# Optimization experiments

Measured on AMD Instinct MI355X. Metric: run time of the kernel, lower is better.

The kernel has to match this reference:

```python
import jax, jax.numpy as jnp
import numpy as np

N = 50000        # nodes
E = 800000       # edges (before self-loops)
IN = 512         # in_channels
HEADS = 8        # 'head' arg: heads and per-head out dim of conv1
C1 = 8           # per-head channels of conv1 (== head)
OUT = 128        # out_channels of conv2
NEG_SLOPE = 0.2  # PyG GATConv leaky-relu slope


def _glorot(key, shape, fan_in):
    return jax.random.normal(key, shape, jnp.float32) * (1.0 / np.sqrt(fan_in))


def setup_inputs() -> dict:
    key = jax.random.key(0)
    ks = jax.random.split(key, 10)
    x = jax.random.normal(ks[0], (N, IN), jnp.float32)
    edge_index = jax.random.randint(ks[1], (2, E), 0, N, dtype=jnp.int32)
    # conv1: GATConv(IN, C1, heads=HEADS, concat=True)
    W1 = _glorot(ks[2], (IN, HEADS * C1), IN)
    att_src1 = _glorot(ks[3], (HEADS, C1), C1)
    att_dst1 = _glorot(ks[4], (HEADS, C1), C1)
    bias1 = jnp.zeros((HEADS * C1,), jnp.float32)
    # conv2: GATConv(HEADS*C1, OUT, heads=1, concat=False)
    W2 = _glorot(ks[5], (HEADS * C1, OUT), HEADS * C1)
    att_src2 = _glorot(ks[6], (1, OUT), OUT)
    att_dst2 = _glorot(ks[7], (1, OUT), OUT)
    bias2 = jnp.zeros((OUT,), jnp.float32)
    return {"x": x, "edge_index": edge_index,
            "W1": W1, "att_src1": att_src1, "att_dst1": att_dst1, "bias1": bias1,
            "W2": W2, "att_src2": att_src2, "att_dst2": att_dst2, "bias2": bias2}


def gat_conv(x, src, dst, W, a_src, a_dst, bias, heads, concat):
    """PyG GATConv (eval mode, dropout off). src/dst already include self-loops."""
    n = x.shape[0]
    h = (x @ W).reshape(n, heads, -1)                 # [N, H, C]
    s = (h * a_src[None]).sum(-1)                     # [N, H] alpha_src per node
    d = (h * a_dst[None]).sum(-1)                     # [N, H] alpha_dst per node
    alpha = jax.nn.leaky_relu(s[src] + d[dst], NEG_SLOPE)  # [E, H]
    # segment softmax over incoming edges of each destination node
    amax = jax.ops.segment_max(alpha, dst, num_segments=n)  # [N, H]
    amax = jnp.where(jnp.isfinite(amax), amax, 0.0)
    ea = jnp.exp(alpha - amax[dst])                   # [E, H]
    denom = jax.ops.segment_sum(ea, dst, num_segments=n)
    w = ea / (denom[dst] + 1e-16)                     # [E, H]
    msg = h[src] * w[..., None]                       # [E, H, C]
    out = jax.ops.segment_sum(msg, dst, num_segments=n)  # [N, H, C]
    out = out.reshape(n, -1) if concat else out.mean(axis=1)
    return out + bias


def reference(x, edge_index, W1, att_src1, att_dst1, bias1,
              W2, att_src2, att_dst2, bias2):
    n = x.shape[0]
    loop = jnp.arange(n, dtype=edge_index.dtype)      # PyG adds self-loops
    src = jnp.concatenate([edge_index[0], loop])
    dst = jnp.concatenate([edge_index[1], loop])
    h = jax.nn.elu(gat_conv(x, src, dst, W1, att_src1, att_dst1, bias1,
                            heads=HEADS, concat=True))
    out = jax.nn.elu(gat_conv(h, src, dst, W2, att_src2, att_dst2, bias2,
                              heads=1, concat=False))
    return out
```

## Files before the change

kernel.cpp:

```cpp
#include <hip/hip_runtime.h>

#define NEG_SLOPE 0.2f

typedef __attribute__((ext_vector_type(8))) short bf16x8;
typedef __attribute__((ext_vector_type(4))) float f32x4;

__device__ __forceinline__ float leaky(float v) {
    return v > 0.0f ? v : NEG_SLOPE * v;
}
__device__ __forceinline__ float elu(float v) {
    return v > 0.0f ? v : (__expf(v) - 1.0f);
}
__device__ __forceinline__ short f2b(float f) {
    return (short)((__float_as_uint(f) + 0x8000u) >> 16);
}
__device__ __forceinline__ float bf2f(unsigned short v) {
    return __uint_as_float(((unsigned)v) << 16);
}

__global__ void prep_k(const float* __restrict__ W1, const float* __restrict__ W2,
                       unsigned short* __restrict__ w1s, unsigned short* __restrict__ w2s,
                       int* __restrict__ deg, int N) {
    int i = blockIdx.x * 256 + threadIdx.x;
    if (i < N) deg[i] = 0;
    if (i < 512 * 64) {
        int k = i >> 6, n = i & 63;
        int kt = k >> 5, kk = k & 31;
        int nt = n >> 4, nn = n & 15;
        int lane = (kk >> 3) * 16 + nn, j = kk & 7;
        w1s[(((size_t)(kt * 4 + nt)) * 64 + lane) * 8 + j] = (unsigned short)f2b(W1[i]);
    } else if (i < 512 * 64 + 64 * 128) {
        int i2 = i - 512 * 64;
        int k = i2 >> 7, n = i2 & 127;
        int kt = k >> 5, kk = k & 31;
        int nt = n >> 4, nn = n & 15;
        int lane = (kk >> 3) * 16 + nn, j = kk & 7;
        w2s[(((size_t)(kt * 8 + nt)) * 64 + lane) * 8 + j] = (unsigned short)f2b(W2[i2]);
    }
}

__global__ __launch_bounds__(256) void gemm1_k(const float* __restrict__ X,
                                               const unsigned short* __restrict__ Ws,
                                               const float* __restrict__ Asrc,
                                               const float* __restrict__ Adst,
                                               unsigned short* __restrict__ Hb,
                                               float* __restrict__ S,
                                               float* __restrict__ D, int N) {
    const int lane = threadIdx.x & 63;
    const int wave = threadIdx.x >> 6;
    const int m0 = blockIdx.x * 64 + wave * 16;
    const int q = lane >> 4, lc = lane & 15;
    const int arow = m0 + lc;
    const float* xrow = X + (size_t)min(arow, N - 1) * 512 + q * 8;
    const bf16x8* bW = (const bf16x8*)Ws;

    f32x4 acc[4] = {{0.f,0.f,0.f,0.f},{0.f,0.f,0.f,0.f},{0.f,0.f,0.f,0.f},{0.f,0.f,0.f,0.f}};

    for (int kt = 0; kt < 16; ++kt) {
        float4 a0 = *(const float4*)(xrow + kt * 32);
        float4 a1 = *(const float4*)(xrow + kt * 32 + 4);
        bf16x8 af;
        af[0] = f2b(a0.x); af[1] = f2b(a0.y); af[2] = f2b(a0.z); af[3] = f2b(a0.w);
        af[4] = f2b(a1.x); af[5] = f2b(a1.y); af[6] = f2b(a1.z); af[7] = f2b(a1.w);
#pragma unroll
        for (int nt = 0; nt < 4; ++nt) {
            bf16x8 bf = bW[(size_t)(kt * 4 + nt) * 64 + lane];
            acc[nt] = __builtin_amdgcn_mfma_f32_16x16x32_bf16(af, bf, acc[nt], 0, 0, 0);
        }
    }

    float asc[4], adc[4];
#pragma unroll
    for (int nt = 0; nt < 4; ++nt) { asc[nt] = Asrc[nt * 16 + lc]; adc[nt] = Adst[nt * 16 + lc]; }

#pragma unroll
    for (int r = 0; r < 4; ++r) {
        int row = m0 + q * 4 + r;
        bool ok = row < N;
        if (ok) {
#pragma unroll
            for (int nt = 0; nt < 4; ++nt)
                Hb[(size_t)row * 64 + nt * 16 + lc] = (unsigned short)f2b(acc[nt][r]);
        }
        float ps[4], pd[4];
#pragma unroll
        for (int nt = 0; nt < 4; ++nt) { ps[nt] = acc[nt][r] * asc[nt]; pd[nt] = acc[nt][r] * adc[nt]; }
#pragma unroll
        for (int off = 1; off < 8; off <<= 1) {
#pragma unroll
            for (int nt = 0; nt < 4; ++nt) {
                ps[nt] += __shfl_xor(ps[nt], off);
                pd[nt] += __shfl_xor(pd[nt], off);
            }
        }
        if (ok && !(lc & 7)) {
            int hb = lc >> 3;
#pragma unroll
            for (int nt = 0; nt < 4; ++nt) {
                S[(size_t)row * 8 + nt * 2 + hb] = ps[nt];
                D[(size_t)row * 8 + nt * 2 + hb] = pd[nt];
            }
        }
    }
}

__global__ __launch_bounds__(256) void gemm2_k(const unsigned short* __restrict__ X,
                                               const unsigned short* __restrict__ Ws,
                                               const float* __restrict__ Asrc,
                                               const float* __restrict__ Adst,
                                               unsigned short* __restrict__ Hb,
                                               float* __restrict__ S,
                                               float* __restrict__ D, int N) {
    const int lane = threadIdx.x & 63;
    const int wave = threadIdx.x >> 6;
    const int m0 = blockIdx.x * 64 + wave * 16;
    const int q = lane >> 4, lc = lane & 15;
    const int arow = m0 + lc;
    const unsigned short* xrow = X + (size_t)min(arow, N - 1) * 64 + q * 8;
    const bf16x8* bW = (const bf16x8*)Ws;

    f32x4 acc[8] = {{0.f,0.f,0.f,0.f},{0.f,0.f,0.f,0.f},{0.f,0.f,0.f,0.f},{0.f,0.f,0.f,0.f},
                    {0.f,0.f,0.f,0.f},{0.f,0.f,0.f,0.f},{0.f,0.f,0.f,0.f},{0.f,0.f,0.f,0.f}};

#pragma unroll
    for (int kt = 0; kt < 2; ++kt) {
        bf16x8 af = *(const bf16x8*)(xrow + kt * 32);
#pragma unroll
        for (int nt = 0; nt < 8; ++nt) {
            bf16x8 bf = bW[(size_t)(kt * 8 + nt) * 64 + lane];
            acc[nt] = __builtin_amdgcn_mfma_f32_16x16x32_bf16(af, bf, acc[nt], 0, 0, 0);
        }
    }

    float asc[8], adc[8];
#pragma unroll
    for (int nt = 0; nt < 8; ++nt) { asc[nt] = Asrc[nt * 16 + lc]; adc[nt] = Adst[nt * 16 + lc]; }

#pragma unroll
    for (int r = 0; r < 4; ++r) {
        int row = m0 + q * 4 + r;
        bool ok = row < N;
        if (ok) {
#pragma unroll
            for (int nt = 0; nt < 8; ++nt)
                Hb[(size_t)row * 128 + nt * 16 + lc] = (unsigned short)f2b(acc[nt][r]);
        }
        float ps = 0.f, pd = 0.f;
#pragma unroll
        for (int nt = 0; nt < 8; ++nt) { ps += acc[nt][r] * asc[nt]; pd += acc[nt][r] * adc[nt]; }
#pragma unroll
        for (int off = 1; off < 16; off <<= 1) {
            ps += __shfl_xor(ps, off);
            pd += __shfl_xor(pd, off);
        }
        if (ok && lc == 0) { S[row] = ps; D[row] = pd; }
    }
}

__global__ void deg_k(const int* __restrict__ dst, int E, int* __restrict__ deg) {
    int base = (blockIdx.x * blockDim.x + threadIdx.x) * 8;
    if (base + 8 <= E) {
        int4 a = *(const int4*)(dst + base);
        int4 b = *(const int4*)(dst + base + 4);
        atomicAdd(&deg[a.x], 1); atomicAdd(&deg[a.y], 1);
        atomicAdd(&deg[a.z], 1); atomicAdd(&deg[a.w], 1);
        atomicAdd(&deg[b.x], 1); atomicAdd(&deg[b.y], 1);
        atomicAdd(&deg[b.z], 1); atomicAdd(&deg[b.w], 1);
    } else {
        for (int e = base; e < E; ++e) atomicAdd(&deg[dst[e]], 1);
    }
}

__global__ __launch_bounds__(256) void scanA_k(const int* __restrict__ deg,
                                               int* __restrict__ rowptr,
                                               int* __restrict__ partials, int N) {
    __shared__ int s[256];
    const int t = threadIdx.x;
    const int base = blockIdx.x * 1024;
    int v[4];
    int idx = base + t * 4;
#pragma unroll
    for (int i = 0; i < 4; ++i) v[i] = (idx + i < N) ? deg[idx + i] + 1 : 0;
    int sum = v[0] + v[1] + v[2] + v[3];
    s[t] = sum;
    __syncthreads();
    for (int off = 1; off < 256; off <<= 1) {
        int x = (t >= off) ? s[t - off] : 0;
        __syncthreads();
        s[t] += x;
        __syncthreads();
    }
    int run = s[t] - sum;
#pragma unroll
    for (int i = 0; i < 4; ++i) {
        if (idx + i < N) rowptr[idx + i] = run;
        run += v[i];
    }
    if (t == 255) partials[blockIdx.x] = s[255];
}

__global__ __launch_bounds__(256) void scanB_k(const int* __restrict__ partials,
                                               int* __restrict__ poff,
                                               int* __restrict__ rowptr, int nb,
                                               int N, int Etot) {
    __shared__ int s[256];
    const int t = threadIdx.x;
    int v = (t < nb) ? partials[t] : 0;
    s[t] = v;
    __syncthreads();
    for (int off = 1; off < 256; off <<= 1) {
        int x = (t >= off) ? s[t - off] : 0;
        __syncthreads();
        s[t] += x;
        __syncthreads();
    }
    poff[t] = s[t] - v;
    if (t == 0) rowptr[N] = Etot;
}

__global__ void scanC_k(int* __restrict__ rowptr, const int* __restrict__ poff,
                        int* __restrict__ wp, int* __restrict__ srcs, int N) {
    int i = blockIdx.x * blockDim.x + threadIdx.x;
    if (i >= N) return;
    int r = rowptr[i] + poff[i >> 10];
    rowptr[i] = r;
    srcs[r] = i;
    wp[i] = r + 1;
}

__global__ void scatter_k(const int* __restrict__ ei, int E,
                          int* __restrict__ wp, int* __restrict__ srcs) {
    int base = (blockIdx.x * blockDim.x + threadIdx.x) * 4;
    if (base + 4 <= E) {
        int4 s = *(const int4*)(ei + base);
        int4 d = *(const int4*)(ei + E + base);
        int p0 = atomicAdd(&wp[d.x], 1);
        int p1 = atomicAdd(&wp[d.y], 1);
        int p2 = atomicAdd(&wp[d.z], 1);
        int p3 = atomicAdd(&wp[d.w], 1);
        srcs[p0] = s.x; srcs[p1] = s.y; srcs[p2] = s.z; srcs[p3] = s.w;
    } else {
        for (int e = base; e < E; ++e) {
            int p = atomicAdd(&wp[ei[E + e]], 1);
            srcs[p] = ei[e];
        }
    }
}

__global__ __launch_bounds__(256) void agg1_csr_k(const int* __restrict__ rowptr,
                                                  const int* __restrict__ srcs,
                                                  const float* __restrict__ S,
                                                  const float* __restrict__ D,
                                                  const unsigned short* __restrict__ Hb,
                                                  const float* __restrict__ bias,
                                                  unsigned short* __restrict__ out, int N) {
    const int wid = (blockIdx.x * 256 + threadIdx.x) >> 6;
    const int lane = threadIdx.x & 63;
    if (wid >= N) return;
    const int beg = rowptr[wid], end = rowptr[wid + 1];
    const int h = lane & 7;
    const int el = lane >> 3;
    const float dvh = D[(size_t)wid * 8 + h];

    float m = -1e30f;
    for (int i = beg + el; i < end; i += 8)
        m = fmaxf(m, leaky(S[(size_t)srcs[i] * 8 + h] + dvh));
#pragma unroll
    for (int off = 8; off < 64; off <<= 1)
        m = fmaxf(m, __shfl_xor(m, off));

    float acc = 0.0f, den = 0.0f;
    for (int base = beg; base < end; base += 8) {
        int i = base + el;
        int src_l = 0; float w_l = 0.0f;
        if (i < end) {
            src_l = srcs[i];
            w_l = __expf(leaky(S[(size_t)src_l * 8 + h] + dvh) - m);
        }
        den += w_l;
#pragma unroll
        for (int j = 0; j < 8; ++j) {
            float w = __shfl(w_l, j * 8 + (lane >> 3));
            int src = __builtin_amdgcn_readfirstlane(__shfl(src_l, j * 8));
            acc += w * bf2f(Hb[(size_t)src * 64 + lane]);
        }
    }
#pragma unroll
    for (int off = 8; off < 64; off <<= 1)
        den += __shfl_xor(den, off);
    float rden = 1.0f / (__shfl(den, lane >> 3) + 1e-16f);
    out[(size_t)wid * 64 + lane] = (unsigned short)f2b(elu(acc * rden + bias[lane]));
}

__global__ __launch_bounds__(256) void agg2_csr_k(const int* __restrict__ rowptr,
                                                  const int* __restrict__ srcs,
                                                  const float* __restrict__ S,
                                                  const float* __restrict__ D,
                                                  const unsigned short* __restrict__ Hb,
                                                  const float* __restrict__ bias,
                                                  float* __restrict__ out, int N) {
    const int wid = (blockIdx.x * 256 + threadIdx.x) >> 6;
    const int lane = threadIdx.x & 63;
    if (wid >= N) return;
    const int beg = rowptr[wid], end = rowptr[wid + 1];
    const float dvh = D[wid];
    const int c0 = lane * 2;

    float m = -1e30f;
    for (int i = beg + lane; i < end; i += 64)
        m = fmaxf(m, leaky(S[srcs[i]] + dvh));
#pragma unroll
    for (int off = 1; off < 64; off <<= 1)
        m = fmaxf(m, __shfl_xor(m, off));

    float acc0 = 0.0f, acc1 = 0.0f, den = 0.0f;
    for (int base = beg; base < end; base += 64) {
        int i = base + lane;
        int src_l = 0; float w_l = 0.0f;
        if (i < end) {
            src_l = srcs[i];
            w_l = __expf(leaky(S[src_l] + dvh) - m);
        }
        den += w_l;
        const int cnt = min(64, end - base);
        for (int j0 = 0; j0 < cnt; j0 += 8) {
#pragma unroll
            for (int u = 0; u < 8; ++u) {
                int j = j0 + u;
                float w = __shfl(w_l, j);
                int src = __builtin_amdgcn_readfirstlane(__shfl(src_l, j));
                unsigned p = *(const unsigned*)(Hb + (size_t)src * 128 + c0);
                acc0 += w * __uint_as_float(p << 16);
                acc1 += w * __uint_as_float(p & 0xffff0000u);
            }
        }
    }
#pragma unroll
    for (int off = 1; off < 64; off <<= 1)
        den += __shfl_xor(den, off);
    const float rden = 1.0f / (den + 1e-16f);
    float2 o;
    o.x = elu(acc0 * rden + bias[c0]);
    o.y = elu(acc1 * rden + bias[c0 + 1]);
    *(float2*)(out + (size_t)wid * 128 + c0) = o;
}

extern "C" void kernel_launch(void* const* d_in, const int* in_sizes, int n_in,
                              void* d_out, int out_size, void* d_ws, size_t ws_size,
                              hipStream_t stream) {
    const float* x   = (const float*)d_in[0];
    const int*   ei  = (const int*)d_in[1];
    const float* W1  = (const float*)d_in[2];
    const float* as1 = (const float*)d_in[3];
    const float* ad1 = (const float*)d_in[4];
    const float* b1  = (const float*)d_in[5];
    const float* W2  = (const float*)d_in[6];
    const float* as2 = (const float*)d_in[7];
    const float* ad2 = (const float*)d_in[8];
    const float* b2  = (const float*)d_in[9];

    const int N = in_sizes[0] / 512;
    const int E = in_sizes[1] / 2;
    const int Etot = E + N;
    float* out = (float*)d_out;

    unsigned short* w1s    = (unsigned short*)d_ws;
    unsigned short* w2s    = w1s + 512 * 64;
    unsigned short* out1b  = w2s + 64 * 128;
    unsigned short* h1b    = out1b + (size_t)N * 64;
    float*          s1     = (float*)(h1b + (size_t)N * 64);
    float*          d1     = s1 + (size_t)N * 8;
    unsigned short* h2b    = (unsigned short*)(d1 + (size_t)N * 8);
    float*          s2     = (float*)(h2b + (size_t)N * 128);
    float*          d2     = s2 + N;
    int*            rowptr = (int*)(d2 + N);
    int*            srcs   = rowptr + (N + 1);
    int* deg      = (int*)h2b;
    int* wp       = deg + N;
    int* partials = wp + N;
    int* poff     = partials + 256;

    const int B = 256;
    const int nb = (N + 1023) / 1024;
    const int gblk = (N + 63) / 64;
    const int prep_n = (N > 512 * 64 + 64 * 128) ? N : (512 * 64 + 64 * 128);

    prep_k<<<(prep_n + B - 1) / B, B, 0, stream>>>(W1, W2, w1s, w2s, deg, N);
    deg_k<<<(E + B * 8 - 1) / (B * 8), B, 0, stream>>>(ei + E, E, deg);
    scanA_k<<<nb, B, 0, stream>>>(deg, rowptr, partials, N);
    scanB_k<<<1, B, 0, stream>>>(partials, poff, rowptr, nb, N, Etot);
    scanC_k<<<(N + B - 1) / B, B, 0, stream>>>(rowptr, poff, wp, srcs, N);
    scatter_k<<<(E + B * 4 - 1) / (B * 4), B, 0, stream>>>(ei, E, wp, srcs);

    gemm1_k<<<gblk, B, 0, stream>>>(x, w1s, as1, ad1, h1b, s1, d1, N);
    agg1_csr_k<<<(N + 3) / 4, B, 0, stream>>>(rowptr, srcs, s1, d1, h1b, b1, out1b, N);

    gemm2_k<<<gblk, B, 0, stream>>>(out1b, w2s, as2, ad2, h2b, s2, d2, N);
    agg2_csr_k<<<(N + 3) / 4, B, 0, stream>>>(rowptr, srcs, s2, d2, h2b, b2, out, N);
}
```

Baseline: 364.8 us.

## Restructure GAT aggregation to per-lane edge groups with 16-byte row loads

Both aggregation kernels now give each lane group its own edge and have each lane load 8 bf16 features with one vector load. This replaces the earlier scheme where every edge was broadcast through shuffles and readfirstlane and each lane loaded one or two elements. Partial sums are combined with a cross-group shuffle reduction at the end, and only one group writes vectorized output. The row max is now taken over raw source scores with leaky applied once afterwards, which is valid because leaky is monotonic. In exchange, each lane holds 8 accumulators and the end of each node pays extra shuffle reductions.

```diff
diff --git a/kernel.cpp b/kernel.cpp
--- a/kernel.cpp
+++ b/kernel.cpp
@@ -259,37 +259,45 @@
     if (wid >= N) return;
     const int beg = rowptr[wid], end = rowptr[wid + 1];
     const int h = lane & 7;
-    const int el = lane >> 3;
+    const int eg = lane >> 3;
     const float dvh = D[(size_t)wid * 8 + h];
 
-    float m = -1e30f;
-    for (int i = beg + el; i < end; i += 8)
-        m = fmaxf(m, leaky(S[(size_t)srcs[i] * 8 + h] + dvh));
+    float ms = -1e30f;
+    for (int i = beg + eg; i < end; i += 8)
+        ms = fmaxf(ms, S[(size_t)srcs[i] * 8 + h]);
 #pragma unroll
     for (int off = 8; off < 64; off <<= 1)
-        m = fmaxf(m, __shfl_xor(m, off));
-
-    float acc = 0.0f, den = 0.0f;
+        ms = fmaxf(ms, __shfl_xor(ms, off));
+    const float m = leaky(ms + dvh);
+
+    float acc[8] = {0.f,0.f,0.f,0.f,0.f,0.f,0.f,0.f};
+    float den = 0.0f;
     for (int base = beg; base < end; base += 8) {
-        int i = base + el;
-        int src_l = 0; float w_l = 0.0f;
-        if (i < end) {
-            src_l = srcs[i];
-            w_l = __expf(leaky(S[(size_t)src_l * 8 + h] + dvh) - m);
-        }
-        den += w_l;
-#pragma unroll
-        for (int j = 0; j < 8; ++j) {
-            float w = __shfl(w_l, j * 8 + (lane >> 3));
-            int src = __builtin_amdgcn_readfirstlane(__shfl(src_l, j * 8));
-            acc += w * bf2f(Hb[(size_t)src * 64 + lane]);
-        }
-    }
-#pragma unroll
-    for (int off = 8; off < 64; off <<= 1)
+        int i = base + eg;
+        bool v = i < end;
+        int src = v ? srcs[i] : wid;
+        float w = v ? __expf(leaky(S[(size_t)src * 8 + h] + dvh) - m) : 0.0f;
+        den += w;
+        bf16x8 hv = *(const bf16x8*)(Hb + (size_t)src * 64 + h * 8);
+#pragma unroll
+        for (int c = 0; c < 8; ++c)
+            acc[c] += w * bf2f((unsigned short)hv[c]);
+    }
+#pragma unroll
+    for (int off = 8; off < 64; off <<= 1) {
         den += __shfl_xor(den, off);
-    float rden = 1.0f / (__shfl(den, lane >> 3) + 1e-16f);
-    out[(size_t)wid * 64 + lane] = (unsigned short)f2b(elu(acc * rden + bias[lane]));
+#pragma unroll
+        for (int c = 0; c < 8; ++c)
+            acc[c] += __shfl_xor(acc[c], off);
+    }
+    if (eg == 0) {
+        const float rden = 1.0f / (den + 1e-16f);
+        bf16x8 o;
+#pragma unroll
+        for (int c = 0; c < 8; ++c)
+            o[c] = f2b(elu(acc[c] * rden + bias[h * 8 + c]));
+        *(bf16x8*)(out + (size_t)wid * 64 + h * 8) = o;
+    }
 }
 
 __global__ __launch_bounds__(256) void agg2_csr_k(const int* __restrict__ rowptr,
@@ -303,46 +311,54 @@
     const int lane = threadIdx.x & 63;
     if (wid >= N) return;
     const int beg = rowptr[wid], end = rowptr[wid + 1];
-    const float dvh = D[wid];
-    const int c0 = lane * 2;
-
-    float m = -1e30f;
+    const int eg = lane >> 4;
+    const int sl = lane & 15;
+    const float dv = D[wid];
+
+    float ms = -1e30f;
     for (int i = beg + lane; i < end; i += 64)
-        m = fmaxf(m, leaky(S[srcs[i]] + dvh));
+        ms = fmaxf(ms, S[srcs[i]]);
 #pragma unroll
     for (int off = 1; off < 64; off <<= 1)
-        m = fmaxf(m, __shfl_xor(m, off));
-
-    float acc0 = 0.0f, acc1 = 0.0f, den = 0.0f;
-    for (int base = beg; base < end; base += 64) {
-        int i = base + lane;
-        int src_l = 0; float w_l = 0.0f;
-        if (i < end) {
-            src_l = srcs[i];
-            w_l = __expf(leaky(S[src_l] + dvh) - m);
-        }
-        den += w_l;
-        const int cnt = min(64, end - base);
-        for (int j0 = 0; j0 < cnt; j0 += 8) {
-#pragma unroll
-            for (int u = 0; u < 8; ++u) {
-                int j = j0 + u;
-                float w = __shfl(w_l, j);
-                int src = __builtin_amdgcn_readfirstlane(__shfl(src_l, j));
-                unsigned p = *(const unsigned*)(Hb + (size_t)src * 128 + c0);
-                acc0 += w * __uint_as_float(p << 16);
-                acc1 += w * __uint_as_float(p & 0xffff0000u);
-            }
-        }
+        ms = fmaxf(ms, __shfl_xor(ms, off));
+    const float m = leaky(ms + dv);
+
+    float acc[8] = {0.f,0.f,0.f,0.f,0.f,0.f,0.f,0.f};
+    float den = 0.0f;
+    for (int base = beg; base < end; base += 4) {
+        int i = base + eg;
+        bool v = i < end;
+        int src = v ? srcs[i] : wid;
+        float w = v ? __expf(leaky(S[src] + dv) - m) : 0.0f;
+        den += w;
+        bf16x8 hv = *(const bf16x8*)(Hb + (size_t)src * 128 + sl * 8);
+#pragma unroll
+        for (int c = 0; c < 8; ++c)
+            acc[c] += w * bf2f((unsigned short)hv[c]);
     }
 #pragma unroll
     for (int off = 1; off < 64; off <<= 1)
         den += __shfl_xor(den, off);
-    const float rden = 1.0f / (den + 1e-16f);
-    float2 o;
-    o.x = elu(acc0 * rden + bias[c0]);
-    o.y = elu(acc1 * rden + bias[c0 + 1]);
-    *(float2*)(out + (size_t)wid * 128 + c0) = o;
+#pragma unroll
+    for (int off = 16; off < 64; off <<= 1) {
+#pragma unroll
+        for (int c = 0; c < 8; ++c)
+            acc[c] += __shfl_xor(acc[c], off);
+    }
+    if (eg == 0) {
+        const float rden = 1.0f / (den * 0.0625f + 1e-16f);
+        float4 o0, o1;
+        o0.x = elu(acc[0] * rden + bias[sl * 8 + 0]);
+        o0.y = elu(acc[1] * rden + bias[sl * 8 + 1]);
+        o0.z = elu(acc[2] * rden + bias[sl * 8 + 2]);
+        o0.w = elu(acc[3] * rden + bias[sl * 8 + 3]);
+        o1.x = elu(acc[4] * rden + bias[sl * 8 + 4]);
+        o1.y = elu(acc[5] * rden + bias[sl * 8 + 5]);
+        o1.z = elu(acc[6] * rden + bias[sl * 8 + 6]);
+        o1.w = elu(acc[7] * rden + bias[sl * 8 + 7]);
+        *(float4*)(out + (size_t)wid * 128 + sl * 8) = o0;
+        *(float4*)(out + (size_t)wid * 128 + sl * 8 + 4) = o1;
+    }
 }
 
 extern "C" void kernel_launch(void* const* d_in, const int* in_sizes, int n_in,
```

After: 378.0 us. 3.6% more time.

## Fuse whole GAT pipeline into one persistent cooperative kernel with grid syncs

Applied to the files above, without the earlier changes.

Replaces the ten separate kernel launches with one persistent cooperative kernel that steps through phases separated by grid.sync, sized from occupancy. The degree count is overlapped with the first GEMM in the same phase. The three-kernel scan is collapsed into one pass that takes chunk offsets with an atomic, and rowptr becomes beg plus deg. The aim is to remove launch gaps and tail effects, at the cost of grid-wide barriers, a fixed persistent grid that may limit latency hiding in the gather phases, and a launch_bounds of 4 that may constrain registers.

```diff
diff --git a/kernel.cpp b/kernel.cpp
--- a/kernel.cpp
+++ b/kernel.cpp
@@ -1,4 +1,7 @@
 #include <hip/hip_runtime.h>
+#include <hip/hip_cooperative_groups.h>
+
+namespace cg = cooperative_groups;
 
 #define NEG_SLOPE 0.2f
 
@@ -18,331 +21,312 @@
     return __uint_as_float(((unsigned)v) << 16);
 }
 
-__global__ void prep_k(const float* __restrict__ W1, const float* __restrict__ W2,
-                       unsigned short* __restrict__ w1s, unsigned short* __restrict__ w2s,
-                       int* __restrict__ deg, int N) {
-    int i = blockIdx.x * 256 + threadIdx.x;
-    if (i < N) deg[i] = 0;
-    if (i < 512 * 64) {
-        int k = i >> 6, n = i & 63;
-        int kt = k >> 5, kk = k & 31;
-        int nt = n >> 4, nn = n & 15;
-        int lane = (kk >> 3) * 16 + nn, j = kk & 7;
-        w1s[(((size_t)(kt * 4 + nt)) * 64 + lane) * 8 + j] = (unsigned short)f2b(W1[i]);
-    } else if (i < 512 * 64 + 64 * 128) {
-        int i2 = i - 512 * 64;
-        int k = i2 >> 7, n = i2 & 127;
-        int kt = k >> 5, kk = k & 31;
-        int nt = n >> 4, nn = n & 15;
-        int lane = (kk >> 3) * 16 + nn, j = kk & 7;
-        w2s[(((size_t)(kt * 8 + nt)) * 64 + lane) * 8 + j] = (unsigned short)f2b(W2[i2]);
-    }
-}
-
-__global__ __launch_bounds__(256) void gemm1_k(const float* __restrict__ X,
-                                               const unsigned short* __restrict__ Ws,
-                                               const float* __restrict__ Asrc,
-                                               const float* __restrict__ Adst,
-                                               unsigned short* __restrict__ Hb,
-                                               float* __restrict__ S,
-                                               float* __restrict__ D, int N) {
-    const int lane = threadIdx.x & 63;
-    const int wave = threadIdx.x >> 6;
-    const int m0 = blockIdx.x * 64 + wave * 16;
-    const int q = lane >> 4, lc = lane & 15;
-    const int arow = m0 + lc;
-    const float* xrow = X + (size_t)min(arow, N - 1) * 512 + q * 8;
-    const bf16x8* bW = (const bf16x8*)Ws;
-
-    f32x4 acc[4] = {{0.f,0.f,0.f,0.f},{0.f,0.f,0.f,0.f},{0.f,0.f,0.f,0.f},{0.f,0.f,0.f,0.f}};
-
-    for (int kt = 0; kt < 16; ++kt) {
-        float4 a0 = *(const float4*)(xrow + kt * 32);
-        float4 a1 = *(const float4*)(xrow + kt * 32 + 4);
-        bf16x8 af;
-        af[0] = f2b(a0.x); af[1] = f2b(a0.y); af[2] = f2b(a0.z); af[3] = f2b(a0.w);
-        af[4] = f2b(a1.x); af[5] = f2b(a1.y); af[6] = f2b(a1.z); af[7] = f2b(a1.w);
-#pragma unroll
-        for (int nt = 0; nt < 4; ++nt) {
-            bf16x8 bf = bW[(size_t)(kt * 4 + nt) * 64 + lane];
-            acc[nt] = __builtin_amdgcn_mfma_f32_16x16x32_bf16(af, bf, acc[nt], 0, 0, 0);
+struct GP {
+    const float* x; const int* ei;
+    const float* W1; const float* as1; const float* ad1; const float* b1;
+    const float* W2; const float* as2; const float* ad2; const float* b2;
+    unsigned short* w1s; unsigned short* w2s;
+    unsigned short* out1b; unsigned short* h1b; unsigned short* h2b;
+    float* s1; float* d1; float* s2; float* d2;
+    int* beg; int* deg; int* wp; int* srcs;
+    float* out;
+    int N; int E;
+};
+
+__global__ __launch_bounds__(256, 4) void fused_k(GP p, int plo, int phi) {
+    cg::grid_group grid = cg::this_grid();
+    const int tid  = threadIdx.x;
+    const int bid  = blockIdx.x;
+    const int nB   = gridDim.x;
+    const int gsz  = nB * 256;
+    const int gtid = bid * 256 + tid;
+    const int lane = tid & 63;
+    const int wave = tid >> 6;
+    const int N = p.N, E = p.E;
+    const int gblk = (N + 63) >> 6;
+    const int nb   = (N + 1023) >> 10;
+    const int nW   = gsz >> 6;
+    const int gw   = gtid >> 6;
+
+    __shared__ int sm[256];
+    __shared__ int chunkBase;
+
+    for (int ph = plo; ph <= phi; ++ph) {
+        switch (ph) {
+        case 0: {
+            for (int i = gtid; i < 512 * 64 + 64 * 128; i += gsz) {
+                if (i < 512 * 64) {
+                    int k = i >> 6, n = i & 63;
+                    int kt = k >> 5, kk = k & 31;
+                    int nt = n >> 4, nn = n & 15;
+                    int l = (kk >> 3) * 16 + nn, j = kk & 7;
+                    p.w1s[(((size_t)(kt * 4 + nt)) * 64 + l) * 8 + j] = (unsigned short)f2b(p.W1[i]);
+                } else {
+                    int i2 = i - 512 * 64;
+                    int k = i2 >> 7, n = i2 & 127;
+                    int kt = k >> 5, kk = k & 31;
+                    int nt = n >> 4, nn = n & 15;
+                    int l = (kk >> 3) * 16 + nn, j = kk & 7;
+                    p.w2s[(((size_t)(kt * 8 + nt)) * 64 + l) * 8 + j] = (unsigned short)f2b(p.W2[i2]);
+                }
+            }
+            for (int i = gtid; i <= N; i += gsz) p.deg[i] = 0;
+        } break;
+
+        case 1: {
+            for (int base = gtid * 8; base < E; base += gsz * 8) {
+                if (base + 8 <= E) {
+                    int4 a = *(const int4*)(p.ei + E + base);
+                    int4 b = *(const int4*)(p.ei + E + base + 4);
+                    atomicAdd(&p.deg[a.x], 1); atomicAdd(&p.deg[a.y], 1);
+                    atomicAdd(&p.deg[a.z], 1); atomicAdd(&p.deg[a.w], 1);
+                    atomicAdd(&p.deg[b.x], 1); atomicAdd(&p.deg[b.y], 1);
+                    atomicAdd(&p.deg[b.z], 1); atomicAdd(&p.deg[b.w], 1);
+                } else {
+                    for (int e = base; e < E; ++e) atomicAdd(&p.deg[p.ei[E + e]], 1);
+                }
+            }
+            const int q = lane >> 4, lc = lane & 15;
+            const bf16x8* bW = (const bf16x8*)p.w1s;
+            for (int t = bid; t < gblk; t += nB) {
+                const int m0 = t * 64 + wave * 16;
+                const int arow = m0 + lc;
+                const float* xrow = p.x + (size_t)min(arow, N - 1) * 512 + q * 8;
+
+                f32x4 acc[4] = {{0.f,0.f,0.f,0.f},{0.f,0.f,0.f,0.f},{0.f,0.f,0.f,0.f},{0.f,0.f,0.f,0.f}};
+                for (int kt = 0; kt < 16; ++kt) {
+                    float4 a0 = *(const float4*)(xrow + kt * 32);
+                    float4 a1 = *(const float4*)(xrow + kt * 32 + 4);
+                    bf16x8 af;
+                    af[0] = f2b(a0.x); af[1] = f2b(a0.y); af[2] = f2b(a0.z); af[3] = f2b(a0.w);
+                    af[4] = f2b(a1.x); af[5] = f2b(a1.y); af[6] = f2b(a1.z); af[7] = f2b(a1.w);
+#pragma unroll
+                    for (int nt = 0; nt < 4; ++nt) {
+                        bf16x8 bf = bW[(size_t)(kt * 4 + nt) * 64 + lane];
+                        acc[nt] = __builtin_amdgcn_mfma_f32_16x16x32_bf16(af, bf, acc[nt], 0, 0, 0);
+                    }
+                }
+                float asc[4], adc[4];
+#pragma unroll
+                for (int nt = 0; nt < 4; ++nt) { asc[nt] = p.as1[nt * 16 + lc]; adc[nt] = p.ad1[nt * 16 + lc]; }
+#pragma unroll
+                for (int r = 0; r < 4; ++r) {
+                    int row = m0 + q * 4 + r;
+                    bool ok = row < N;
+                    if (ok) {
+#pragma unroll
+                        for (int nt = 0; nt < 4; ++nt)
+                            p.h1b[(size_t)row * 64 + nt * 16 + lc] = (unsigned short)f2b(acc[nt][r]);
+                    }
+                    float ps[4], pd[4];
+#pragma unroll
+                    for (int nt = 0; nt < 4; ++nt) { ps[nt] = acc[nt][r] * asc[nt]; pd[nt] = acc[nt][r] * adc[nt]; }
+#pragma unroll
+                    for (int off = 1; off < 8; off <<= 1) {
+#pragma unroll
+                        for (int nt = 0; nt < 4; ++nt) {
+                            ps[nt] += __shfl_xor(ps[nt], off);
+                            pd[nt] += __shfl_xor(pd[nt], off);
+                        }
+                    }
+                    if (ok && !(lc & 7)) {
+                        int hb = lc >> 3;
+#pragma unroll
+                        for (int nt = 0; nt < 4; ++nt) {
+                            p.s1[(size_t)row * 8 + nt * 2 + hb] = ps[nt];
+                            p.d1[(size_t)row * 8 + nt * 2 + hb] = pd[nt];
+                        }
+                    }
+                }
+            }
+        } break;
+
+        case 2: {
+            for (int c = nB - 1 - bid; c < nb; c += nB) {
+                int v[4];
+                int idx = c * 1024 + tid * 4;
+#pragma unroll
+                for (int i = 0; i < 4; ++i) v[i] = (idx + i < N) ? p.deg[idx + i] + 1 : 0;
+                int sum = v[0] + v[1] + v[2] + v[3];
+                sm[tid] = sum;
+                __syncthreads();
+                for (int off = 1; off < 256; off <<= 1) {
+                    int xv = (tid >= off) ? sm[tid - off] : 0;
+                    __syncthreads();
+                    sm[tid] += xv;
+                    __syncthreads();
+                }
+                if (tid == 255) chunkBase = atomicAdd(&p.deg[N], sm[255]);
+                __syncthreads();
+                int run = chunkBase + sm[tid] - sum;
+#pragma unroll
+                for (int i = 0; i < 4; ++i) {
+                    if (idx + i < N) {
+                        p.beg[idx + i] = run;
+                        p.srcs[run] = idx + i;
+                        p.wp[idx + i] = run + 1;
+                        run += v[i];
+                    }
+                }
+                __syncthreads();
+            }
+        } break;
+
+        case 3: {
+            for (int base = gtid * 4; base < E; base += gsz * 4) {
+                if (base + 4 <= E) {
+                    int4 s = *(const int4*)(p.ei + base);
+                    int4 d = *(const int4*)(p.ei + E + base);
+                    int p0 = atomicAdd(&p.wp[d.x], 1);
+                    int p1 = atomicAdd(&p.wp[d.y], 1);
+                    int p2 = atomicAdd(&p.wp[d.z], 1);
+                    int p3 = atomicAdd(&p.wp[d.w], 1);
+                    p.srcs[p0] = s.x; p.srcs[p1] = s.y; p.srcs[p2] = s.z; p.srcs[p3] = s.w;
+                } else {
+                    for (int e = base; e < E; ++e) {
+                        int pp = atomicAdd(&p.wp[p.ei[E + e]], 1);
+                        p.srcs[pp] = p.ei[e];
+                    }
+                }
+            }
+        } break;
+
+        case 4: {
+            for (int wid = gw; wid < N; wid += nW) {
+                const int b0 = p.beg[wid];
+                const int e0 = b0 + p.deg[wid] + 1;
+                const int h = lane & 7;
+                const int el = lane >> 3;
+                const float dvh = p.d1[(size_t)wid * 8 + h];
+
+                float m = -1e30f;
+                for (int i = b0 + el; i < e0; i += 8)
+                    m = fmaxf(m, leaky(p.s1[(size_t)p.srcs[i] * 8 + h] + dvh));
+#pragma unroll
+                for (int off = 8; off < 64; off <<= 1)
+                    m = fmaxf(m, __shfl_xor(m, off));
+
+                float acc = 0.0f, den = 0.0f;
+                for (int base = b0; base < e0; base += 8) {
+                    int i = base + el;
+                    int src_l = 0; float w_l = 0.0f;
+                    if (i < e0) {
+                        src_l = p.srcs[i];
+                        w_l = __expf(leaky(p.s1[(size_t)src_l * 8 + h] + dvh) - m);
+                    }
+                    den += w_l;
+#pragma unroll
+                    for (int j = 0; j < 8; ++j) {
+                        float w = __shfl(w_l, j * 8 + (lane >> 3));
+                        int src = __builtin_amdgcn_readfirstlane(__shfl(src_l, j * 8));
+                        acc += w * bf2f(p.h1b[(size_t)src * 64 + lane]);
+                    }
+                }
+#pragma unroll
+                for (int off = 8; off < 64; off <<= 1)
+                    den += __shfl_xor(den, off);
+                float rden = 1.0f / (__shfl(den, lane >> 3) + 1e-16f);
+                p.out1b[(size_t)wid * 64 + lane] = (unsigned short)f2b(elu(acc * rden + p.b1[lane]));
+            }
+        } break;
+
+        case 5: {
+            const int q = lane >> 4, lc = lane & 15;
+            const bf16x8* bW = (const bf16x8*)p.w2s;
+            for (int t = bid; t < gblk; t += nB) {
+                const int m0 = t * 64 + wave * 16;
+                const int arow = m0 + lc;
+                const unsigned short* xrow = p.out1b + (size_t)min(arow, N - 1) * 64 + q * 8;
+
+                f32x4 acc[8] = {{0.f,0.f,0.f,0.f},{0.f,0.f,0.f,0.f},{0.f,0.f,0.f,0.f},{0.f,0.f,0.f,0.f},
+                                {0.f,0.f,0.f,0.f},{0.f,0.f,0.f,0.f},{0.f,0.f,0.f,0.f},{0.f,0.f,0.f,0.f}};
+#pragma unroll
+                for (int kt = 0; kt < 2; ++kt) {
+                    bf16x8 af = *(const bf16x8*)(xrow + kt * 32);
+#pragma unroll
+                    for (int nt = 0; nt < 8; ++nt) {
+                        bf16x8 bf = bW[(size_t)(kt * 8 + nt) * 64 + lane];
+                        acc[nt] = __builtin_amdgcn_mfma_f32_16x16x32_bf16(af, bf, acc[nt], 0, 0, 0);
+                    }
+                }
+                float asc[8], adc[8];
+#pragma unroll
+                for (int nt = 0; nt < 8; ++nt) { asc[nt] = p.as2[nt * 16 + lc]; adc[nt] = p.ad2[nt * 16 + lc]; }
+#pragma unroll
+                for (int r = 0; r < 4; ++r) {
+                    int row = m0 + q * 4 + r;
+                    bool ok = row < N;
+                    if (ok) {
+#pragma unroll
+                        for (int nt = 0; nt < 8; ++nt)
+                            p.h2b[(size_t)row * 128 + nt * 16 + lc] = (unsigned short)f2b(acc[nt][r]);
+                    }
+                    float ps = 0.f, pd = 0.f;
+#pragma unroll
+                    for (int nt = 0; nt < 8; ++nt) { ps += acc[nt][r] * asc[nt]; pd += acc[nt][r] * adc[nt]; }
+#pragma unroll
+                    for (int off = 1; off < 16; off <<= 1) {
+                        ps += __shfl_xor(ps, off);
+                        pd += __shfl_xor(pd, off);
+                    }
+                    if (ok && lc == 0) { p.s2[row] = ps; p.d2[row] = pd; }
+                }
+            }
+        } break;
+
+        case 6: {
+            for (int wid = gw; wid < N; wid += nW) {
+                const int b0 = p.beg[wid];
+                const int e0 = b0 + p.deg[wid] + 1;
+                const float dv = p.d2[wid];
+                const int c0 = lane * 2;
+
+                float m = -1e30f;
+                for (int i = b0 + lane; i < e0; i += 64)
+                    m = fmaxf(m, leaky(p.s2[p.srcs[i]] + dv));
+#pragma unroll
+                for (int off = 1; off < 64; off <<= 1)
+                    m = fmaxf(m, __shfl_xor(m, off));
+
+                float acc0 = 0.0f, acc1 = 0.0f, den = 0.0f;
+                for (int base = b0; base < e0; base += 64) {
+                    int i = base + lane;
+                    int src_l = 0; float w_l = 0.0f;
+                    if (i < e0) {
+                        src_l = p.srcs[i];
+                        w_l = __expf(leaky(p.s2[src_l] + dv) - m);
+                    }
+                    den += w_l;
+                    const int cnt = min(64, e0 - base);
+                    for (int j0 = 0; j0 < cnt; j0 += 8) {
+#pragma unroll
+                        for (int u = 0; u < 8; ++u) {
+                            int j = j0 + u;
+                            float w = __shfl(w_l, j);
+                            int src = __builtin_amdgcn_readfirstlane(__shfl(src_l, j));
+                            unsigned pv = *(const unsigned*)(p.h2b + (size_t)src * 128 + c0);
+                            acc0 += w * __uint_as_float(pv << 16);
+                            acc1 += w * __uint_as_float(pv & 0xffff0000u);
+                        }
+                    }
+                }
+#pragma unroll
+                for (int off = 1; off < 64; off <<= 1)
+                    den += __shfl_xor(den, off);
+                const float rden = 1.0f / (den + 1e-16f);
+                float2 o;
+                o.x = elu(acc0 * rden + p.b2[c0]);
+                o.y = elu(acc1 * rden + p.b2[c0 + 1]);
+                *(float2*)(p.out + (size_t)wid * 128 + c0) = o;
+            }
+        } break;
+        }
+
+        if (ph < phi) {
+            __threadfence();
+            grid.sync();
         }
     }
-
-    float asc[4], adc[4];
-#pragma unroll
-    for (int nt = 0; nt < 4; ++nt) { asc[nt] = Asrc[nt * 16 + lc]; adc[nt] = Adst[nt * 16 + lc]; }
-
-#pragma unroll
-    for (int r = 0; r < 4; ++r) {
-        int row = m0 + q * 4 + r;
-        bool ok = row < N;
-        if (ok) {
-#pragma unroll
-            for (int nt = 0; nt < 4; ++nt)
-                Hb[(size_t)row * 64 + nt * 16 + lc] = (unsigned short)f2b(acc[nt][r]);
-        }
-        float ps[4], pd[4];
-#pragma unroll
-        for (int nt = 0; nt < 4; ++nt) { ps[nt] = acc[nt][r] * asc[nt]; pd[nt] = acc[nt][r] * adc[nt]; }
-#pragma unroll
-        for (int off = 1; off < 8; off <<= 1) {
-#pragma unroll
-            for (int nt = 0; nt < 4; ++nt) {
-                ps[nt] += __shfl_xor(ps[nt], off);
-                pd[nt] += __shfl_xor(pd[nt], off);
-            }
-        }
-        if (ok && !(lc & 7)) {
-            int hb = lc >> 3;
-#pragma unroll
-            for (int nt = 0; nt < 4; ++nt) {
-                S[(size_t)row * 8 + nt * 2 + hb] = ps[nt];
-                D[(size_t)row * 8 + nt * 2 + hb] = pd[nt];
-            }
-        }
-    }
-}
-
-__global__ __launch_bounds__(256) void gemm2_k(const unsigned short* __restrict__ X,
-                                               const unsigned short* __restrict__ Ws,
-                                               const float* __restrict__ Asrc,
-                                               const float* __restrict__ Adst,
-                                               unsigned short* __restrict__ Hb,
-                                               float* __restrict__ S,
-                                               float* __restrict__ D, int N) {
-    const int lane = threadIdx.x & 63;
-    const int wave = threadIdx.x >> 6;
-    const int m0 = blockIdx.x * 64 + wave * 16;
-    const int q = lane >> 4, lc = lane & 15;
-    const int arow = m0 + lc;
-    const unsigned short* xrow = X + (size_t)min(arow, N - 1) * 64 + q * 8;
-    const bf16x8* bW = (const bf16x8*)Ws;
-
-    f32x4 acc[8] = {{0.f,0.f,0.f,0.f},{0.f,0.f,0.f,0.f},{0.f,0.f,0.f,0.f},{0.f,0.f,0.f,0.f},
-                    {0.f,0.f,0.f,0.f},{0.f,0.f,0.f,0.f},{0.f,0.f,0.f,0.f},{0.f,0.f,0.f,0.f}};
-
-#pragma unroll
-    for (int kt = 0; kt < 2; ++kt) {
-        bf16x8 af = *(const bf16x8*)(xrow + kt * 32);
-#pragma unroll
-        for (int nt = 0; nt < 8; ++nt) {
-            bf16x8 bf = bW[(size_t)(kt * 8 + nt) * 64 + lane];
-            acc[nt] = __builtin_amdgcn_mfma_f32_16x16x32_bf16(af, bf, acc[nt], 0, 0, 0);
-        }
-    }
-
-    float asc[8], adc[8];
-#pragma unroll
-    for (int nt = 0; nt < 8; ++nt) { asc[nt] = Asrc[nt * 16 + lc]; adc[nt] = Adst[nt * 16 + lc]; }
-
-#pragma unroll
-    for (int r = 0; r < 4; ++r) {
-        int row = m0 + q * 4 + r;
-        bool ok = row < N;
-        if (ok) {
-#pragma unroll
-            for (int nt = 0; nt < 8; ++nt)
-                Hb[(size_t)row * 128 + nt * 16 + lc] = (unsigned short)f2b(acc[nt][r]);
-        }
-        float ps = 0.f, pd = 0.f;
-#pragma unroll
-        for (int nt = 0; nt < 8; ++nt) { ps += acc[nt][r] * asc[nt]; pd += acc[nt][r] * adc[nt]; }
-#pragma unroll
-        for (int off = 1; off < 16; off <<= 1) {
-            ps += __shfl_xor(ps, off);
-            pd += __shfl_xor(pd, off);
-        }
-        if (ok && lc == 0) { S[row] = ps; D[row] = pd; }
-    }
-}
-
-__global__ void deg_k(const int* __restrict__ dst, int E, int* __restrict__ deg) {
-    int base = (blockIdx.x * blockDim.x + threadIdx.x) * 8;
-    if (base + 8 <= E) {
-        int4 a = *(const int4*)(dst + base);
-        int4 b = *(const int4*)(dst + base + 4);
-        atomicAdd(&deg[a.x], 1); atomicAdd(&deg[a.y], 1);
-        atomicAdd(&deg[a.z], 1); atomicAdd(&deg[a.w], 1);
-        atomicAdd(&deg[b.x], 1); atomicAdd(&deg[b.y], 1);
-        atomicAdd(&deg[b.z], 1); atomicAdd(&deg[b.w], 1);
-    } else {
-        for (int e = base; e < E; ++e) atomicAdd(&deg[dst[e]], 1);
-    }
-}
-
-__global__ __launch_bounds__(256) void scanA_k(const int* __restrict__ deg,
-                                               int* __restrict__ rowptr,
-                                               int* __restrict__ partials, int N) {
-    __shared__ int s[256];
-    const int t = threadIdx.x;
-    const int base = blockIdx.x * 1024;
-    int v[4];
-    int idx = base + t * 4;
-#pragma unroll
-    for (int i = 0; i < 4; ++i) v[i] = (idx + i < N) ? deg[idx + i] + 1 : 0;
-    int sum = v[0] + v[1] + v[2] + v[3];
-    s[t] = sum;
-    __syncthreads();
-    for (int off = 1; off < 256; off <<= 1) {
-        int x = (t >= off) ? s[t - off] : 0;
-        __syncthreads();
-        s[t] += x;
-        __syncthreads();
-    }
-    int run = s[t] - sum;
-#pragma unroll
-    for (int i = 0; i < 4; ++i) {
-        if (idx + i < N) rowptr[idx + i] = run;
-        run += v[i];
-    }
-    if (t == 255) partials[blockIdx.x] = s[255];
-}
-
-__global__ __launch_bounds__(256) void scanB_k(const int* __restrict__ partials,
-                                               int* __restrict__ poff,
-                                               int* __restrict__ rowptr, int nb,
-                                               int N, int Etot) {
-    __shared__ int s[256];
-    const int t = threadIdx.x;
-    int v = (t < nb) ? partials[t] : 0;
-    s[t] = v;
-    __syncthreads();
-    for (int off = 1; off < 256; off <<= 1) {
-        int x = (t >= off) ? s[t - off] : 0;
-        __syncthreads();
-        s[t] += x;
-        __syncthreads();
-    }
-    poff[t] = s[t] - v;
-    if (t == 0) rowptr[N] = Etot;
-}
-
-__global__ void scanC_k(int* __restrict__ rowptr, const int* __restrict__ poff,
-                        int* __restrict__ wp, int* __restrict__ srcs, int N) {
-    int i = blockIdx.x * blockDim.x + threadIdx.x;
-    if (i >= N) return;
-    int r = rowptr[i] + poff[i >> 10];
-    rowptr[i] = r;
-    srcs[r] = i;
-    wp[i] = r + 1;
-}
-
-__global__ void scatter_k(const int* __restrict__ ei, int E,
-                          int* __restrict__ wp, int* __restrict__ srcs) {
-    int base = (blockIdx.x * blockDim.x + threadIdx.x) * 4;
-    if (base + 4 <= E) {
-        int4 s = *(const int4*)(ei + base);
-        int4 d = *(const int4*)(ei + E + base);
-        int p0 = atomicAdd(&wp[d.x], 1);
-        int p1 = atomicAdd(&wp[d.y], 1);
-        int p2 = atomicAdd(&wp[d.z], 1);
-        int p3 = atomicAdd(&wp[d.w], 1);
-        srcs[p0] = s.x; srcs[p1] = s.y; srcs[p2] = s.z; srcs[p3] = s.w;
-    } else {
-        for (int e = base; e < E; ++e) {
-            int p = atomicAdd(&wp[ei[E + e]], 1);
-            srcs[p] = ei[e];
-        }
-    }
-}
-
-__global__ __launch_bounds__(256) void agg1_csr_k(const int* __restrict__ rowptr,
-                                                  const int* __restrict__ srcs,
-                                                  const float* __restrict__ S,
-                                                  const float* __restrict__ D,
-                                                  const unsigned short* __restrict__ Hb,
-                                                  const float* __restrict__ bias,
-                                                  unsigned short* __restrict__ out, int N) {
-    const int wid = (blockIdx.x * 256 + threadIdx.x) >> 6;
-    const int lane = threadIdx.x & 63;
-    if (wid >= N) return;
-    const int beg = rowptr[wid], end = rowptr[wid + 1];
-    const int h = lane & 7;
-    const int el = lane >> 3;
-    const float dvh = D[(size_t)wid * 8 + h];
-
-    float m = -1e30f;
-    for (int i = beg + el; i < end; i += 8)
-        m = fmaxf(m, leaky(S[(size_t)srcs[i] * 8 + h] + dvh));
-#pragma unroll
-    for (int off = 8; off < 64; off <<= 1)
-        m = fmaxf(m, __shfl_xor(m, off));
-
-    float acc = 0.0f, den = 0.0f;
-    for (int base = beg; base < end; base += 8) {
-        int i = base + el;
-        int src_l = 0; float w_l = 0.0f;
-        if (i < end) {
-            src_l = srcs[i];
-            w_l = __expf(leaky(S[(size_t)src_l * 8 + h] + dvh) - m);
-        }
-        den += w_l;
-#pragma unroll
-        for (int j = 0; j < 8; ++j) {
-            float w = __shfl(w_l, j * 8 + (lane >> 3));
-            int src = __builtin_amdgcn_readfirstlane(__shfl(src_l, j * 8));
-            acc += w * bf2f(Hb[(size_t)src * 64 + lane]);
-        }
-    }
-#pragma unroll
-    for (int off = 8; off < 64; off <<= 1)
-        den += __shfl_xor(den, off);
-    float rden = 1.0f / (__shfl(den, lane >> 3) + 1e-16f);
-    out[(size_t)wid * 64 + lane] = (unsigned short)f2b(elu(acc * rden + bias[lane]));
-}
-
-__global__ __launch_bounds__(256) void agg2_csr_k(const int* __restrict__ rowptr,
-                                                  const int* __restrict__ srcs,
-                                                  const float* __restrict__ S,
-                                                  const float* __restrict__ D,
-                                                  const unsigned short* __restrict__ Hb,
-                                                  const float* __restrict__ bias,
-                                                  float* __restrict__ out, int N) {
-    const int wid = (blockIdx.x * 256 + threadIdx.x) >> 6;
-    const int lane = threadIdx.x & 63;
-    if (wid >= N) return;
-    const int beg = rowptr[wid], end = rowptr[wid + 1];
-    const float dvh = D[wid];
-    const int c0 = lane * 2;
-
-    float m = -1e30f;
-    for (int i = beg + lane; i < end; i += 64)
-        m = fmaxf(m, leaky(S[srcs[i]] + dvh));
-#pragma unroll
-    for (int off = 1; off < 64; off <<= 1)
-        m = fmaxf(m, __shfl_xor(m, off));
-
-    float acc0 = 0.0f, acc1 = 0.0f, den = 0.0f;
-    for (int base = beg; base < end; base += 64) {
-        int i = base + lane;
-        int src_l = 0; float w_l = 0.0f;
-        if (i < end) {
-            src_l = srcs[i];
-            w_l = __expf(leaky(S[src_l] + dvh) - m);
-        }
-        den += w_l;
-        const int cnt = min(64, end - base);
-        for (int j0 = 0; j0 < cnt; j0 += 8) {
-#pragma unroll
-            for (int u = 0; u < 8; ++u) {
-                int j = j0 + u;
-                float w = __shfl(w_l, j);
-                int src = __builtin_amdgcn_readfirstlane(__shfl(src_l, j));
-                unsigned p = *(const unsigned*)(Hb + (size_t)src * 128 + c0);
-                acc0 += w * __uint_as_float(p << 16);
-                acc1 += w * __uint_as_float(p & 0xffff0000u);
-            }
-        }
-    }
-#pragma unroll
-    for (int off = 1; off < 64; off <<= 1)
-        den += __shfl_xor(den, off);
-    const float rden = 1.0f / (den + 1e-16f);
-    float2 o;
-    o.x = elu(acc0 * rden + bias[c0]);
-    o.y = elu(acc1 * rden + bias[c0 + 1]);
-    *(float2*)(out + (size_t)wid * 128 + c0) = o;
 }
 
 extern "C" void kernel_launch(void* const* d_in, const int* in_sizes, int n_in,
@@ -361,40 +345,57 @@
 
     const int N = in_sizes[0] / 512;
     const int E = in_sizes[1] / 2;
-    const int Etot = E + N;
-    float* out = (float*)d_out;
-
-    unsigned short* w1s    = (unsigned short*)d_ws;
-    unsigned short* w2s    = w1s + 512 * 64;
-    unsigned short* out1b  = w2s + 64 * 128;
-    unsigned short* h1b    = out1b + (size_t)N * 64;
-    float*          s1     = (float*)(h1b + (size_t)N * 64);
-    float*          d1     = s1 + (size_t)N * 8;
-    unsigned short* h2b    = (unsigned short*)(d1 + (size_t)N * 8);
-    float*          s2     = (float*)(h2b + (size_t)N * 128);
-    float*          d2     = s2 + N;
-    int*            rowptr = (int*)(d2 + N);
-    int*            srcs   = rowptr + (N + 1);
-    int* deg      = (int*)h2b;
-    int* wp       = deg + N;
-    int* partials = wp + N;
-    int* poff     = partials + 256;
-
-    const int B = 256;
-    const int nb = (N + 1023) / 1024;
-    const int gblk = (N + 63) / 64;
-    const int prep_n = (N > 512 * 64 + 64 * 128) ? N : (512 * 64 + 64 * 128);
-
-    prep_k<<<(prep_n + B - 1) / B, B, 0, stream>>>(W1, W2, w1s, w2s, deg, N);
-    deg_k<<<(E + B * 8 - 1) / (B * 8), B, 0, stream>>>(ei + E, E, deg);
-    scanA_k<<<nb, B, 0, stream>>>(deg, rowptr, partials, N);
-    scanB_k<<<1, B, 0, stream>>>(partials, poff, rowptr, nb, N, Etot);
-    scanC_k<<<(N + B - 1) / B, B, 0, stream>>>(rowptr, poff, wp, srcs, N);
-    scatter_k<<<(E + B * 4 - 1) / (B * 4), B, 0, stream>>>(ei, E, wp, srcs);
-
-    gemm1_k<<<gblk, B, 0, stream>>>(x, w1s, as1, ad1, h1b, s1, d1, N);
-    agg1_csr_k<<<(N + 3) / 4, B, 0, stream>>>(rowptr, srcs, s1, d1, h1b, b1, out1b, N);
-
-    gemm2_k<<<gblk, B, 0, stream>>>(out1b, w2s, as2, ad2, h2b, s2, d2, N);
-    agg2_csr_k<<<(N + 3) / 4, B, 0, stream>>>(rowptr, srcs, s2, d2, h2b, b2, out, N);
-}
+
+    unsigned short* w1s   = (unsigned short*)d_ws;
+    unsigned short* w2s   = w1s + 512 * 64;
+    unsigned short* out1b = w2s + 64 * 128;
+    unsigned short* h1b   = out1b + (size_t)N * 64;
+    unsigned short* h2b   = h1b + (size_t)N * 64;
+    float*          s1    = (float*)(h2b + (size_t)N * 128);
+    float*          d1    = s1 + (size_t)N * 8;
+    float*          s2    = d1 + (size_t)N * 8;
+    float*          d2    = s2 + N;
+    int*            beg   = (int*)(d2 + N);
+    int*            deg   = beg + N;
+    int*            wp    = deg + (N + 1);
+    int*            srcs  = wp + N;
+
+    GP p;
+    p.x = x; p.ei = ei;
+    p.W1 = W1; p.as1 = as1; p.ad1 = ad1; p.b1 = b1;
+    p.W2 = W2; p.as2 = as2; p.ad2 = ad2; p.b2 = b2;
+    p.w1s = w1s; p.w2s = w2s; p.out1b = out1b; p.h1b = h1b; p.h2b = h2b;
+    p.s1 = s1; p.d1 = d1; p.s2 = s2; p.d2 = d2;
+    p.beg = beg; p.deg = deg; p.wp = wp; p.srcs = srcs;
+    p.out = (float*)d_out;
+    p.N = N; p.E = E;
+
+    static int coop_blocks = []() -> int {
+        int dev = 0;
+        if (hipGetDevice(&dev) != hipSuccess) dev = 0;
+        hipDeviceProp_t props;
+        int cus = 256;
+        if (hipGetDeviceProperties(&props, dev) == hipSuccess && props.multiProcessorCount > 0)
+            cus = props.multiProcessorCount;
+        int maxb = 0;
+        if (hipOccupancyMaxActiveBlocksPerMultiprocessor(&maxb, fused_k, 256, 0) != hipSuccess)
+            maxb = 0;
+        if (maxb <= 0) return 0;
+        long g = (long)cus * maxb;
+        if (g > 2048) g = 2048;
+        return (int)g;
+    }();
+
+    hipError_t err = hipErrorUnknown;
+    if (coop_blocks > 0) {
+        int lo = 0, hi = 6;
+        void* args[] = { &p, &lo, &hi };
+        err = hipLaunchCooperativeKernel((const void*)fused_k, dim3(coop_blocks), dim3(256),
+                                         args, 0, stream);
+    }
+    if (err != hipSuccess) {
+        (void)hipGetLastError();
+        for (int ph = 0; ph <= 6; ++ph)
+            hipLaunchKernelGGL(fused_k, dim3(1024), dim3(256), 0, stream, p, ph, ph);
+    }
+}
```

After: 1.277 ms. 3.5x slower.
